# Kernel tuning notes

Measured on AMD Instinct MI355X. Metric: run time of the kernel, lower is better.

The kernel has to match this reference:

```python
import jax, jax.numpy as jnp
import numpy as np

B, S, DIM, HEADS, DHEAD = 1, 1992, 2048, 16, 128
NKI_SEQ_ALIGN = 128
EPS = 1e-6


def setup_inputs() -> dict:
    key = jax.random.key(0)
    ks = jax.random.split(key, 8)
    hidden_states = jax.random.normal(ks[0], (B, S, DIM), dtype=jnp.float32)
    # realistic rotary tables, full head_dim with interleaved pair angles
    pos = jnp.arange(S, dtype=jnp.float32)
    inv_freq = 1.0 / (10000.0 ** (jnp.arange(0, DHEAD, 2, dtype=jnp.float32) / DHEAD))
    ang = pos[:, None] * inv_freq[None, :]                      # [S, DHEAD/2]
    full = jnp.stack([ang, ang], axis=-1).reshape(S, DHEAD)     # interleave
    freqs_cos = jnp.cos(full)[None, :, None, :]                 # [1,S,1,DHEAD]
    freqs_sin = jnp.sin(full)[None, :, None, :]
    sc = 0.02
    wq = jax.random.normal(ks[1], (DIM, DIM), dtype=jnp.float32) * sc
    wk = jax.random.normal(ks[2], (DIM, DIM), dtype=jnp.float32) * sc
    wv = jax.random.normal(ks[3], (DIM, DIM), dtype=jnp.float32) * sc
    wo = jax.random.normal(ks[4], (DIM, DIM), dtype=jnp.float32) * sc
    bq = jax.random.normal(ks[5], (DIM,), dtype=jnp.float32) * sc
    bk = jax.random.normal(ks[6], (DIM,), dtype=jnp.float32) * sc
    bv = jax.random.normal(ks[7], (DIM,), dtype=jnp.float32) * sc
    bo = jnp.zeros((DIM,), dtype=jnp.float32)
    norm_q_w = jnp.ones((DIM,), dtype=jnp.float32)
    norm_k_w = jnp.ones((DIM,), dtype=jnp.float32)
    return dict(hidden_states=hidden_states, freqs_cos=freqs_cos, freqs_sin=freqs_sin,
                wq=wq, bq=bq, wk=wk, bk=bk, wv=wv, bv=bv,
                norm_q_w=norm_q_w, norm_k_w=norm_k_w, wo=wo, bo=bo)


def _rms_norm(x, weight, eps=EPS):
    xf = x.astype(jnp.float32)
    var = jnp.mean(xf * xf, axis=-1, keepdims=True)
    return (weight * (xf * jax.lax.rsqrt(var + eps))).astype(x.dtype)


def _apply_rope(x, freqs_cos, freqs_sin):
    # x: [B,H,S,D]; freqs: [1,S,1,D]
    cos = jnp.transpose(freqs_cos[..., 0::2], (0, 2, 1, 3))  # [1,1,S,D/2]
    sin = jnp.transpose(freqs_sin[..., 1::2], (0, 2, 1, 3))
    x1, x2 = x[..., 0::2], x[..., 1::2]
    o1 = x1 * cos - x2 * sin
    o2 = x1 * sin + x2 * cos
    return jnp.stack([o1, o2], axis=-1).reshape(x.shape)


def _attention_padded(q, k, v):
    # Faithful to nki_flash_attention: zero-pad seq to multiple of 128,
    # no masking of padded keys (they contribute logit 0), trim query pad.
    B_, H_, S_, D_ = q.shape
    pad = (-S_) % NKI_SEQ_ALIGN
    if pad:
        pc = [(0, 0), (0, 0), (0, pad), (0, 0)]
        q = jnp.pad(q, pc); k = jnp.pad(k, pc); v = jnp.pad(v, pc)
    scale = 1.0 / np.sqrt(D_)
    scores = jnp.einsum('bhqd,bhkd->bhqk', q, k) * scale
    probs = jax.nn.softmax(scores, axis=-1)
    out = jnp.einsum('bhqk,bhkd->bhqd', probs, v)
    return out[:, :, :S_, :]


def reference(hidden_states, freqs_cos, freqs_sin, wq, bq, wk, bk, wv, bv,
              norm_q_w, norm_k_w, wo, bo):
    b, s, _ = hidden_states.shape
    q = hidden_states @ wq.T + bq
    k = hidden_states @ wk.T + bk
    v = hidden_states @ wv.T + bv
    q = _rms_norm(q, norm_q_w)
    k = _rms_norm(k, norm_k_w)
    hd = q.shape[-1] // HEADS
    q = q.reshape(b, s, HEADS, hd).transpose(0, 2, 1, 3)
    k = k.reshape(b, s, HEADS, hd).transpose(0, 2, 1, 3)
    v = v.reshape(b, s, HEADS, hd).transpose(0, 2, 1, 3)
    q = _apply_rope(q, freqs_cos, freqs_sin)
    k = _apply_rope(k, freqs_cos, freqs_sin)
    o = _attention_padded(q, k, v)
    o = o.transpose(0, 2, 1, 3).reshape(b, s, -1)
    return o @ wo.T + bo
```

## Files before the change

kernel.cpp:

```cpp
#include <hip/hip_runtime.h>
#include <cstdint>

#define S_REAL 1992
#define S_PAD  2048
#define DIMSZ  2048
#define NHEAD  16
#define DHD    128

typedef float f32x4 __attribute__((ext_vector_type(4)));
typedef __bf16 bf16x8 __attribute__((ext_vector_type(8)));
typedef unsigned short u16x8 __attribute__((ext_vector_type(8)));

__device__ __forceinline__ unsigned short f2bf(float f){
  uint32_t u = __float_as_uint(f);
  u += 0x7fffu + ((u >> 16) & 1u);
  return (unsigned short)(u >> 16);
}

__device__ __forceinline__ void gload16(const void* g, void* l){
  __builtin_amdgcn_global_load_lds(
      (const __attribute__((address_space(1))) uint32_t*)g,
      (__attribute__((address_space(3))) uint32_t*)l,
      16, 0, 0);
}

template<int N> __device__ __forceinline__ void waitbar(){
  if constexpr (N == 8)      asm volatile("s_waitcnt vmcnt(8)\n\ts_barrier" ::: "memory");
  else if constexpr (N == 6) asm volatile("s_waitcnt vmcnt(6)\n\ts_barrier" ::: "memory");
  else if constexpr (N == 4) asm volatile("s_waitcnt vmcnt(4)\n\ts_barrier" ::: "memory");
  else if constexpr (N == 3) asm volatile("s_waitcnt vmcnt(3)\n\ts_barrier" ::: "memory");
  else                       asm volatile("s_waitcnt vmcnt(0)\n\ts_barrier" ::: "memory");
}

__launch_bounds__(256)
__global__ void k_cvt(const float* __restrict__ src, unsigned short* __restrict__ dst, int n8){
  int i = blockIdx.x * 256 + threadIdx.x;
  if (i >= n8) return;
  const float4* s = (const float4*)src + (size_t)i * 2;
  float4 a = s[0], b = s[1];
  u16x8 o;
  o[0]=f2bf(a.x); o[1]=f2bf(a.y); o[2]=f2bf(a.z); o[3]=f2bf(a.w);
  o[4]=f2bf(b.x); o[5]=f2bf(b.y); o[6]=f2bf(b.z); o[7]=f2bf(b.w);
  *((u16x8*)dst + i) = o;
}

template<int BN>
__launch_bounds__(512, 2)
__global__ void k_gemm8(const unsigned short* __restrict__ A,
                        const unsigned short* __restrict__ B0,
                        const unsigned short* __restrict__ B1,
                        const unsigned short* __restrict__ B2,
                        const float* __restrict__ bias0,
                        const float* __restrict__ bias1,
                        const float* __restrict__ bias2,
                        float* __restrict__ C0, float* __restrict__ C1, float* __restrict__ C2,
                        int Mreal)
{
  constexpr int WN   = BN / 64;
  constexpr int RM   = 256 / (8 / WN);
  constexpr int MI   = RM / 16;
  constexpr int NL   = (256 + BN) / 128;
  constexpr int BUFE = (256 + BN) * 32;
  constexpr int NT   = DIMSZ / 32;

  __shared__ unsigned short lds[4 * BUFE];

  const unsigned short* Bm = (blockIdx.z == 0) ? B0 : ((blockIdx.z == 1) ? B1 : B2);
  const float* bias        = (blockIdx.z == 0) ? bias0 : ((blockIdx.z == 1) ? bias1 : bias2);
  float* C                 = (blockIdx.z == 0) ? C0 : ((blockIdx.z == 1) ? C1 : C2);

  const int tid = threadIdx.x;
  const int w = tid >> 6, l = tid & 63;
  const int lr = l & 15, lg = l >> 4;
  const int m0 = blockIdx.x * 256, n0 = blockIdx.y * BN;
  const int wr = (w / WN) * RM, wc = (w % WN) * 64;

  f32x4 acc[MI][4];
  #pragma unroll
  for (int mi = 0; mi < MI; ++mi)
    #pragma unroll
    for (int ni = 0; ni < 4; ++ni)
      acc[mi][ni] = (f32x4){0.f, 0.f, 0.f, 0.f};

#define G8_STAGE(TT) do{                                                          \
    const int k0s = (TT) * 32;                                                    \
    unsigned short* dst = &lds[((TT) & 3) * BUFE];                                \
    _Pragma("unroll")                                                             \
    for (int i_ = 0; i_ < 2; ++i_){                                               \
      int lin = i_ * 512 + tid;                                                   \
      int r_ = lin >> 2, pos_ = lin & 3;                                          \
      int gr_ = m0 + r_; if (gr_ > Mreal - 1) gr_ = Mreal - 1;                    \
      gload16(A + (size_t)gr_ * DIMSZ + k0s + (pos_ ^ ((r_ >> 1) & 3)) * 8,       \
              dst + lin * 8);                                                     \
    }                                                                             \
    _Pragma("unroll")                                                             \
    for (int i_ = 0; i_ < BN / 128; ++i_){                                        \
      int lin = i_ * 512 + tid;                                                   \
      int r_ = lin >> 2, pos_ = lin & 3;                                          \
      gload16(Bm + (size_t)(n0 + r_) * DIMSZ + k0s + (pos_ ^ ((r_ >> 1) & 3)) * 8,\
              dst + 8192 + lin * 8);                                              \
    }                                                                             \
  } while(0)

#define G8_COMPUTE(TT) do{                                                        \
    const unsigned short* sb = &lds[((TT) & 3) * BUFE];                           \
    bf16x8 af_[MI]; bf16x8 bf_[4];                                                \
    _Pragma("unroll")                                                             \
    for (int mi = 0; mi < MI; ++mi){                                              \
      int r_ = wr + mi * 16 + lr;                                                 \
      af_[mi] = *(const bf16x8*)(sb + r_ * 32 + (lg ^ ((r_ >> 1) & 3)) * 8);      \
    }                                                                             \
    _Pragma("unroll")                                                             \
    for (int ni = 0; ni < 4; ++ni){                                               \
      int r_ = wc + ni * 16 + lr;                                                 \
      bf_[ni] = *(const bf16x8*)(sb + 8192 + r_ * 32 + (lg ^ ((r_ >> 1) & 3)) * 8);\
    }                                                                             \
    __builtin_amdgcn_s_setprio(1);                                                \
    _Pragma("unroll")                                                             \
    for (int mi = 0; mi < MI; ++mi)                                               \
      _Pragma("unroll")                                                           \
      for (int ni = 0; ni < 4; ++ni)                                              \
        acc[mi][ni] = __builtin_amdgcn_mfma_f32_16x16x32_bf16(af_[mi], bf_[ni],   \
                                                              acc[mi][ni], 0, 0, 0);\
    __builtin_amdgcn_s_setprio(0);                                                \
  } while(0)

  G8_STAGE(0); G8_STAGE(1); G8_STAGE(2);

  for (int tt = 0; tt < NT - 3; ++tt){
    waitbar<2 * NL>();
    G8_STAGE(tt + 3);
    G8_COMPUTE(tt);
  }
  waitbar<2 * NL>(); G8_COMPUTE(NT - 3);
  waitbar<NL>();     G8_COMPUTE(NT - 2);
  waitbar<0>();      G8_COMPUTE(NT - 1);

#undef G8_STAGE
#undef G8_COMPUTE

  #pragma unroll
  for (int ni = 0; ni < 4; ++ni){
    int col = n0 + wc + ni * 16 + lr;
    float bz = bias[col];
    #pragma unroll
    for (int mi = 0; mi < MI; ++mi){
      #pragma unroll
      for (int j = 0; j < 4; ++j){
        int row = m0 + wr + mi * 16 + lg * 4 + j;
        if (row < Mreal) C[(size_t)row * DIMSZ + col] = acc[mi][ni][j] + bz;
      }
    }
  }
}

__launch_bounds__(256)
__global__ void k_normrope(const float* __restrict__ Xf, const float* __restrict__ nw,
                           const float* __restrict__ fc, const float* __restrict__ fs,
                           unsigned short* __restrict__ Out, float scale, int swz)
{
  const int s = blockIdx.x;
  const int t = threadIdx.x;
  const int w = t >> 6, l = t & 63;
  __shared__ float wred[4];
  float v[8];
  float ss = 0.f;
  if (s < S_REAL){
    const float4* p = (const float4*)(Xf + (size_t)s * DIMSZ) + t * 2;
    float4 a = p[0], b = p[1];
    v[0]=a.x; v[1]=a.y; v[2]=a.z; v[3]=a.w; v[4]=b.x; v[5]=b.y; v[6]=b.z; v[7]=b.w;
    #pragma unroll
    for (int j = 0; j < 8; ++j) ss += v[j] * v[j];
  }
  #pragma unroll
  for (int off = 32; off >= 1; off >>= 1) ss += __shfl_xor(ss, off);
  if (l == 0) wred[w] = ss;
  __syncthreads();
  float tot = wred[0] + wred[1] + wred[2] + wred[3];
  float rinv = rsqrtf(tot * (1.f / DIMSZ) + 1e-6f);

  const int h  = t >> 4;
  const int d0 = (t & 15) * 8;
  const int b  = t & 15;
  const int bsw = swz ? (b ^ (s & 7)) : b;
  unsigned short* dst = Out + ((size_t)h * S_PAD + s) * DHD + bsw * 8;
  u16x8 o;
  if (s < S_REAL){
    #pragma unroll
    for (int i = 0; i < 4; ++i){
      float c_ = fc[s * DHD + d0 + 2 * i];
      float s_ = fs[s * DHD + d0 + 2 * i + 1];
      float x1 = v[2 * i]     * rinv * nw[t * 8 + 2 * i];
      float x2 = v[2 * i + 1] * rinv * nw[t * 8 + 2 * i + 1];
      o[2 * i]     = f2bf((x1 * c_ - x2 * s_) * scale);
      o[2 * i + 1] = f2bf((x1 * s_ + x2 * c_) * scale);
    }
  } else {
    #pragma unroll
    for (int j = 0; j < 8; ++j) o[j] = 0;
  }
  *(u16x8*)dst = o;
}

__launch_bounds__(256)
__global__ void k_vtrans(const float* __restrict__ Vf, unsigned short* __restrict__ Vth)
{
  __shared__ unsigned short tile[64][72];
  const int t = threadIdx.x;
  const int s0 = blockIdx.x * 64, c0 = blockIdx.y * 64;
  #pragma unroll
  for (int i = 0; i < 4; ++i){
    int r = (t >> 4) * 4 + i;
    int s = s0 + r;
    int cq = (t & 15) * 4;
    float4 val = {0.f, 0.f, 0.f, 0.f};
    if (s < S_REAL) val = *((const float4*)(Vf + (size_t)s * DIMSZ + c0) + (t & 15));
    tile[r][cq + 0] = f2bf(val.x);
    tile[r][cq + 1] = f2bf(val.y);
    tile[r][cq + 2] = f2bf(val.z);
    tile[r][cq + 3] = f2bf(val.w);
  }
  __syncthreads();
  const int cl = t >> 2;
  const int cc = c0 + cl;
  #pragma unroll
  for (int bi = 0; bi < 2; ++bi){
    int b = (t & 3) * 2 + bi;
    u16x8 o;
    #pragma unroll
    for (int j = 0; j < 8; ++j) o[j] = tile[b * 8 + j][cl];
    int bsw = b ^ (cc & 7);
    *(u16x8*)(Vth + (size_t)cc * S_PAD + s0 + bsw * 8) = o;
  }
}

__launch_bounds__(256)
__global__ void k_attn(const unsigned short* __restrict__ Qh,
                       const unsigned short* __restrict__ Kh,
                       const unsigned short* __restrict__ Vth,
                       unsigned short* __restrict__ O)
{
  __shared__ unsigned short kbuf[64 * 128];
  __shared__ unsigned short vbuf[128 * 64];
  __shared__ unsigned short pbuf[4][16 * 64];
  const int h = blockIdx.y;
  const int q0 = blockIdx.x * 64;
  const int t = threadIdx.x, w = t >> 6, l = t & 63;
  const int lr = l & 15, lg = l >> 4;

  const unsigned short* Qp = Qh + ((size_t)h * S_PAD + q0 + w * 16 + lr) * DHD;
  bf16x8 qf[4];
  #pragma unroll
  for (int ks = 0; ks < 4; ++ks) qf[ks] = *(const bf16x8*)(Qp + ks * 32 + lg * 8);

  f32x4 acc[8];
  #pragma unroll
  for (int nf = 0; nf < 8; ++nf) acc[nf] = (f32x4){0.f, 0.f, 0.f, 0.f};
  float m[4], lsum[4];
  #pragma unroll
  for (int j = 0; j < 4; ++j){ m[j] = -3.0e38f; lsum[j] = 0.f; }

  for (int kt = 0; kt < S_PAD / 64; ++kt){
    __syncthreads();
    #pragma unroll
    for (int i = 0; i < 4; ++i){
      int rK = (w * 4 + i) * 4 + (l >> 4);
      gload16(Kh + ((size_t)h * S_PAD + kt * 64 + rK) * DHD + (l & 15) * 8, &kbuf[(w * 4 + i) * 512]);
      int rV = (w * 4 + i) * 8 + (l >> 3);
      gload16(Vth + ((size_t)h * DHD + rV) * S_PAD + kt * 64 + (l & 7) * 8, &vbuf[(w * 4 + i) * 512]);
    }
    __syncthreads();

    f32x4 sf[4];
    #pragma unroll
    for (int kvf = 0; kvf < 4; ++kvf){
      sf[kvf] = (f32x4){0.f, 0.f, 0.f, 0.f};
      int r = kvf * 16 + lr;
      #pragma unroll
      for (int ks = 0; ks < 4; ++ks){
        int blk = (ks * 4 + lg) ^ (r & 7);
        bf16x8 kf = *(const bf16x8*)&kbuf[r * 128 + blk * 8];
        sf[kvf] = __builtin_amdgcn_mfma_f32_16x16x32_bf16(qf[ks], kf, sf[kvf], 0, 0, 0);
      }
    }

    float rowmax[4], rowsum[4], fr[4];
    #pragma unroll
    for (int j = 0; j < 4; ++j)
      rowmax[j] = fmaxf(fmaxf(sf[0][j], sf[1][j]), fmaxf(sf[2][j], sf[3][j]));
    #pragma unroll
    for (int off = 1; off <= 8; off <<= 1)
      #pragma unroll
      for (int j = 0; j < 4; ++j) rowmax[j] = fmaxf(rowmax[j], __shfl_xor(rowmax[j], off));
    #pragma unroll
    for (int j = 0; j < 4; ++j){
      float mn = fmaxf(m[j], rowmax[j]);
      fr[j] = __expf(m[j] - mn);
      m[j] = mn;
    }
    float p[4][4];
    #pragma unroll
    for (int kvf = 0; kvf < 4; ++kvf)
      #pragma unroll
      for (int j = 0; j < 4; ++j) p[kvf][j] = __expf(sf[kvf][j] - m[j]);
    #pragma unroll
    for (int j = 0; j < 4; ++j) rowsum[j] = p[0][j] + p[1][j] + p[2][j] + p[3][j];
    #pragma unroll
    for (int off = 1; off <= 8; off <<= 1)
      #pragma unroll
      for (int j = 0; j < 4; ++j) rowsum[j] += __shfl_xor(rowsum[j], off);
    f32x4 fv = (f32x4){fr[0], fr[1], fr[2], fr[3]};
    #pragma unroll
    for (int j = 0; j < 4; ++j) lsum[j] = lsum[j] * fr[j] + rowsum[j];
    #pragma unroll
    for (int nf = 0; nf < 8; ++nf) acc[nf] *= fv;

    unsigned short* pb = pbuf[w];
    #pragma unroll
    for (int kvf = 0; kvf < 4; ++kvf)
      #pragma unroll
      for (int j = 0; j < 4; ++j){
        int r = lg * 4 + j;
        int c = kvf * 16 + lr;
        int blk = (c >> 3) ^ (r & 7);
        pb[r * 64 + blk * 8 + (c & 7)] = f2bf(p[kvf][j]);
      }

    bf16x8 pf[2];
    #pragma unroll
    for (int ks = 0; ks < 2; ++ks){
      int blk = (ks * 4 + lg) ^ (lr & 7);
      pf[ks] = *(const bf16x8*)&pb[lr * 64 + blk * 8];
    }
    #pragma unroll
    for (int nf = 0; nf < 8; ++nf){
      int c = nf * 16 + lr;
      #pragma unroll
      for (int ks = 0; ks < 2; ++ks){
        int blk = (ks * 4 + lg) ^ (c & 7);
        bf16x8 vf = *(const bf16x8*)&vbuf[c * 64 + blk * 8];
        acc[nf] = __builtin_amdgcn_mfma_f32_16x16x32_bf16(pf[ks], vf, acc[nf], 0, 0, 0);
      }
    }
  }

  #pragma unroll
  for (int nf = 0; nf < 8; ++nf){
    #pragma unroll
    for (int j = 0; j < 4; ++j){
      int row = q0 + w * 16 + lg * 4 + j;
      if (row < S_REAL)
        O[(size_t)row * DIMSZ + h * DHD + nf * 16 + lr] = f2bf(acc[nf][j] / lsum[j]);
    }
  }
}

extern "C" void kernel_launch(void* const* d_in, const int* in_sizes, int n_in,
                              void* d_out, int out_size, void* d_ws, size_t ws_size,
                              hipStream_t stream)
{
  const float* hidden = (const float*)d_in[0];
  const float* fc  = (const float*)d_in[1];
  const float* fs  = (const float*)d_in[2];
  const float* wq  = (const float*)d_in[3];
  const float* bq  = (const float*)d_in[4];
  const float* wk  = (const float*)d_in[5];
  const float* bk  = (const float*)d_in[6];
  const float* wv  = (const float*)d_in[7];
  const float* bv  = (const float*)d_in[8];
  const float* nqw = (const float*)d_in[9];
  const float* nkw = (const float*)d_in[10];
  const float* wo  = (const float*)d_in[11];
  const float* bo  = (const float*)d_in[12];
  float* out = (float*)d_out;

  char* ws = (char*)d_ws;
  size_t off = 0;
  auto alloc = [&](size_t bytes) -> void* {
    void* p = ws + off;
    off += (bytes + 255) & ~(size_t)255;
    return p;
  };
  unsigned short* Xb  = (unsigned short*)alloc((size_t)S_REAL * DIMSZ * 2);
  unsigned short* Wqb = (unsigned short*)alloc((size_t)DIMSZ * DIMSZ * 2);
  unsigned short* Wkb = (unsigned short*)alloc((size_t)DIMSZ * DIMSZ * 2);
  unsigned short* Wvb = (unsigned short*)alloc((size_t)DIMSZ * DIMSZ * 2);
  unsigned short* Wob = (unsigned short*)alloc((size_t)DIMSZ * DIMSZ * 2);
  float* Qf = (float*)alloc((size_t)S_REAL * DIMSZ * 4);
  float* Kf = (float*)alloc((size_t)S_REAL * DIMSZ * 4);
  float* Vf = (float*)alloc((size_t)S_REAL * DIMSZ * 4);
  unsigned short* Qhh = (unsigned short*)alloc((size_t)NHEAD * S_PAD * DHD * 2);
  unsigned short* Khh = (unsigned short*)alloc((size_t)NHEAD * S_PAD * DHD * 2);
  unsigned short* Vth = (unsigned short*)alloc((size_t)NHEAD * DHD * S_PAD * 2);
  unsigned short* Oa  = (unsigned short*)alloc((size_t)S_REAL * DIMSZ * 2);

  k_cvt<<<S_REAL * DIMSZ / 8 / 256, 256, 0, stream>>>(hidden, Xb, S_REAL * DIMSZ / 8);
  k_cvt<<<DIMSZ * DIMSZ / 8 / 256, 256, 0, stream>>>(wq, Wqb, DIMSZ * DIMSZ / 8);
  k_cvt<<<DIMSZ * DIMSZ / 8 / 256, 256, 0, stream>>>(wk, Wkb, DIMSZ * DIMSZ / 8);
  k_cvt<<<DIMSZ * DIMSZ / 8 / 256, 256, 0, stream>>>(wv, Wvb, DIMSZ * DIMSZ / 8);
  k_cvt<<<DIMSZ * DIMSZ / 8 / 256, 256, 0, stream>>>(wo, Wob, DIMSZ * DIMSZ / 8);

  k_gemm8<256><<<dim3(8, 8, 3), 512, 0, stream>>>(Xb, Wqb, Wkb, Wvb, bq, bk, bv,
                                                  Qf, Kf, Vf, S_REAL);

  k_normrope<<<S_PAD, 256, 0, stream>>>(Qf, nqw, fc, fs, Qhh, 0.08838834764831843f, 0);
  k_normrope<<<S_PAD, 256, 0, stream>>>(Kf, nkw, fc, fs, Khh, 1.0f, 1);

  k_vtrans<<<dim3(S_PAD / 64, DIMSZ / 64), 256, 0, stream>>>(Vf, Vth);

  k_attn<<<dim3(S_PAD / 64, NHEAD), 256, 0, stream>>>(Qhh, Khh, Vth, Oa);

  k_gemm8<128><<<dim3(8, 16, 1), 512, 0, stream>>>(Oa, Wob, Wob, Wob, bo, bo, bo,
                                                   out, out, out, S_REAL);
}
```

Baseline: 256.0 us.

## Double-buffer attention K/V loads, transpose QK MFMA, retile output GEMM

The attention kernel now double-buffers K and V tiles in shared memory, prefetching the next tile while the current one is computed, so only one barrier per iteration remains. The QK MFMA operands are swapped, which transposes the score layout so each lane owns one query row's max and sum, cutting the shuffle reductions. P is written to LDS with packed 8-byte stores, and MFMA sections get raised priority. The GEMM gains a BM template parameter, and the output projection uses 128x128 tiles over 256 blocks to improve occupancy, at the cost of more redundant loads of A and B.

Result: faster. 218.6 us (-14.6%).

```diff
diff --git a/kernel.cpp b/kernel.cpp
--- a/kernel.cpp
+++ b/kernel.cpp
@@ -29,6 +29,7 @@
   else if constexpr (N == 6) asm volatile("s_waitcnt vmcnt(6)\n\ts_barrier" ::: "memory");
   else if constexpr (N == 4) asm volatile("s_waitcnt vmcnt(4)\n\ts_barrier" ::: "memory");
   else if constexpr (N == 3) asm volatile("s_waitcnt vmcnt(3)\n\ts_barrier" ::: "memory");
+  else if constexpr (N == 2) asm volatile("s_waitcnt vmcnt(2)\n\ts_barrier" ::: "memory");
   else                       asm volatile("s_waitcnt vmcnt(0)\n\ts_barrier" ::: "memory");
 }
 
@@ -44,7 +45,7 @@
   *((u16x8*)dst + i) = o;
 }
 
-template<int BN>
+template<int BM, int BN>
 __launch_bounds__(512, 2)
 __global__ void k_gemm8(const unsigned short* __restrict__ A,
                         const unsigned short* __restrict__ B0,
@@ -57,10 +58,12 @@
                         int Mreal)
 {
   constexpr int WN   = BN / 64;
-  constexpr int RM   = 256 / (8 / WN);
+  constexpr int WM   = 8 / WN;
+  constexpr int RM   = BM / WM;
   constexpr int MI   = RM / 16;
-  constexpr int NL   = (256 + BN) / 128;
-  constexpr int BUFE = (256 + BN) * 32;
+  constexpr int NL   = (BM + BN) / 128;
+  constexpr int BUFE = (BM + BN) * 32;
+  constexpr int BOFF = BM * 32;
   constexpr int NT   = DIMSZ / 32;
 
   __shared__ unsigned short lds[4 * BUFE];
@@ -72,7 +75,7 @@
   const int tid = threadIdx.x;
   const int w = tid >> 6, l = tid & 63;
   const int lr = l & 15, lg = l >> 4;
-  const int m0 = blockIdx.x * 256, n0 = blockIdx.y * BN;
+  const int m0 = blockIdx.x * BM, n0 = blockIdx.y * BN;
   const int wr = (w / WN) * RM, wc = (w % WN) * 64;
 
   f32x4 acc[MI][4];
@@ -86,7 +89,7 @@
     const int k0s = (TT) * 32;                                                    \
     unsigned short* dst = &lds[((TT) & 3) * BUFE];                                \
     _Pragma("unroll")                                                             \
-    for (int i_ = 0; i_ < 2; ++i_){                                               \
+    for (int i_ = 0; i_ < BM / 128; ++i_){                                        \
       int lin = i_ * 512 + tid;                                                   \
       int r_ = lin >> 2, pos_ = lin & 3;                                          \
       int gr_ = m0 + r_; if (gr_ > Mreal - 1) gr_ = Mreal - 1;                    \
@@ -98,7 +101,7 @@
       int lin = i_ * 512 + tid;                                                   \
       int r_ = lin >> 2, pos_ = lin & 3;                                          \
       gload16(Bm + (size_t)(n0 + r_) * DIMSZ + k0s + (pos_ ^ ((r_ >> 1) & 3)) * 8,\
-              dst + 8192 + lin * 8);                                              \
+              dst + BOFF + lin * 8);                                              \
     }                                                                             \
   } while(0)
 
@@ -113,7 +116,7 @@
     _Pragma("unroll")                                                             \
     for (int ni = 0; ni < 4; ++ni){                                               \
       int r_ = wc + ni * 16 + lr;                                                 \
-      bf_[ni] = *(const bf16x8*)(sb + 8192 + r_ * 32 + (lg ^ ((r_ >> 1) & 3)) * 8);\
+      bf_[ni] = *(const bf16x8*)(sb + BOFF + r_ * 32 + (lg ^ ((r_ >> 1) & 3)) * 8);\
     }                                                                             \
     __builtin_amdgcn_s_setprio(1);                                                \
     _Pragma("unroll")                                                             \
@@ -240,8 +243,8 @@
                        const unsigned short* __restrict__ Vth,
                        unsigned short* __restrict__ O)
 {
-  __shared__ unsigned short kbuf[64 * 128];
-  __shared__ unsigned short vbuf[128 * 64];
+  __shared__ unsigned short kbuf[2][64 * 128];
+  __shared__ unsigned short vbuf[2][128 * 64];
   __shared__ unsigned short pbuf[4][16 * 64];
   const int h = blockIdx.y;
   const int q0 = blockIdx.x * 64;
@@ -256,22 +259,29 @@
   f32x4 acc[8];
   #pragma unroll
   for (int nf = 0; nf < 8; ++nf) acc[nf] = (f32x4){0.f, 0.f, 0.f, 0.f};
-  float m[4], lsum[4];
-  #pragma unroll
-  for (int j = 0; j < 4; ++j){ m[j] = -3.0e38f; lsum[j] = 0.f; }
+  float m = -3.0e38f, lsum = 0.f;
+
+#define ATT_STAGE(KT, BI) do{                                                       \
+    _Pragma("unroll")                                                               \
+    for (int i_ = 0; i_ < 4; ++i_){                                                 \
+      int rK = (w * 4 + i_) * 4 + (l >> 4);                                         \
+      gload16(Kh + ((size_t)h * S_PAD + (KT) * 64 + rK) * DHD + (l & 15) * 8,       \
+              &kbuf[BI][(w * 4 + i_) * 512]);                                       \
+      int rV = (w * 4 + i_) * 8 + (l >> 3);                                         \
+      gload16(Vth + ((size_t)h * DHD + rV) * S_PAD + (KT) * 64 + (l & 7) * 8,       \
+              &vbuf[BI][(w * 4 + i_) * 512]);                                       \
+    }                                                                               \
+  } while(0)
+
+  ATT_STAGE(0, 0);
+  __syncthreads();
 
   for (int kt = 0; kt < S_PAD / 64; ++kt){
-    __syncthreads();
-    #pragma unroll
-    for (int i = 0; i < 4; ++i){
-      int rK = (w * 4 + i) * 4 + (l >> 4);
-      gload16(Kh + ((size_t)h * S_PAD + kt * 64 + rK) * DHD + (l & 15) * 8, &kbuf[(w * 4 + i) * 512]);
-      int rV = (w * 4 + i) * 8 + (l >> 3);
-      gload16(Vth + ((size_t)h * DHD + rV) * S_PAD + kt * 64 + (l & 7) * 8, &vbuf[(w * 4 + i) * 512]);
-    }
-    __syncthreads();
+    const int bi = kt & 1;
+    if (kt < S_PAD / 64 - 1) ATT_STAGE(kt + 1, bi ^ 1);
 
     f32x4 sf[4];
+    __builtin_amdgcn_s_setprio(1);
     #pragma unroll
     for (int kvf = 0; kvf < 4; ++kvf){
       sf[kvf] = (f32x4){0.f, 0.f, 0.f, 0.f};
@@ -279,70 +289,76 @@
       #pragma unroll
       for (int ks = 0; ks < 4; ++ks){
         int blk = (ks * 4 + lg) ^ (r & 7);
-        bf16x8 kf = *(const bf16x8*)&kbuf[r * 128 + blk * 8];
-        sf[kvf] = __builtin_amdgcn_mfma_f32_16x16x32_bf16(qf[ks], kf, sf[kvf], 0, 0, 0);
+        bf16x8 kf = *(const bf16x8*)&kbuf[bi][r * 128 + blk * 8];
+        sf[kvf] = __builtin_amdgcn_mfma_f32_16x16x32_bf16(kf, qf[ks], sf[kvf], 0, 0, 0);
       }
     }
-
-    float rowmax[4], rowsum[4], fr[4];
-    #pragma unroll
-    for (int j = 0; j < 4; ++j)
-      rowmax[j] = fmaxf(fmaxf(sf[0][j], sf[1][j]), fmaxf(sf[2][j], sf[3][j]));
-    #pragma unroll
-    for (int off = 1; off <= 8; off <<= 1)
-      #pragma unroll
-      for (int j = 0; j < 4; ++j) rowmax[j] = fmaxf(rowmax[j], __shfl_xor(rowmax[j], off));
-    #pragma unroll
-    for (int j = 0; j < 4; ++j){
-      float mn = fmaxf(m[j], rowmax[j]);
-      fr[j] = __expf(m[j] - mn);
-      m[j] = mn;
-    }
-    float p[4][4];
+    __builtin_amdgcn_s_setprio(0);
+
+    float pmax = sf[0][0];
     #pragma unroll
     for (int kvf = 0; kvf < 4; ++kvf)
       #pragma unroll
-      for (int j = 0; j < 4; ++j) p[kvf][j] = __expf(sf[kvf][j] - m[j]);
-    #pragma unroll
-    for (int j = 0; j < 4; ++j) rowsum[j] = p[0][j] + p[1][j] + p[2][j] + p[3][j];
-    #pragma unroll
-    for (int off = 1; off <= 8; off <<= 1)
-      #pragma unroll
-      for (int j = 0; j < 4; ++j) rowsum[j] += __shfl_xor(rowsum[j], off);
-    f32x4 fv = (f32x4){fr[0], fr[1], fr[2], fr[3]};
-    #pragma unroll
-    for (int j = 0; j < 4; ++j) lsum[j] = lsum[j] * fr[j] + rowsum[j];
-    #pragma unroll
-    for (int nf = 0; nf < 8; ++nf) acc[nf] *= fv;
-
-    unsigned short* pb = pbuf[w];
+      for (int j = 0; j < 4; ++j) pmax = fmaxf(pmax, sf[kvf][j]);
+    pmax = fmaxf(pmax, __shfl_xor(pmax, 16));
+    pmax = fmaxf(pmax, __shfl_xor(pmax, 32));
+    float mn = fmaxf(m, pmax);
+    float fr = __expf(m - mn);
+    m = mn;
+    float p[4][4];
+    float psum = 0.f;
     #pragma unroll
     for (int kvf = 0; kvf < 4; ++kvf)
       #pragma unroll
-      for (int j = 0; j < 4; ++j){
-        int r = lg * 4 + j;
-        int c = kvf * 16 + lr;
-        int blk = (c >> 3) ^ (r & 7);
-        pb[r * 64 + blk * 8 + (c & 7)] = f2bf(p[kvf][j]);
-      }
-
+      for (int j = 0; j < 4; ++j){ p[kvf][j] = __expf(sf[kvf][j] - mn); psum += p[kvf][j]; }
+    lsum = lsum * fr + psum;
+
+    float fv0 = __shfl(fr, lg * 4 + 0);
+    float fv1 = __shfl(fr, lg * 4 + 1);
+    float fv2 = __shfl(fr, lg * 4 + 2);
+    float fv3 = __shfl(fr, lg * 4 + 3);
+    f32x4 fv = (f32x4){fv0, fv1, fv2, fv3};
+    #pragma unroll
+    for (int nf = 0; nf < 8; ++nf) acc[nf] *= fv;
+
+    char* pb = (char*)pbuf[w];
+    #pragma unroll
+    for (int kvf = 0; kvf < 4; ++kvf){
+      uint2 wv;
+      wv.x = (uint32_t)f2bf(p[kvf][0]) | ((uint32_t)f2bf(p[kvf][1]) << 16);
+      wv.y = (uint32_t)f2bf(p[kvf][2]) | ((uint32_t)f2bf(p[kvf][3]) << 16);
+      int byte = lr * 128 + (((kvf * 2 + (lg >> 1)) ^ (lr & 7)) * 16) + (lg & 1) * 8;
+      *(uint2*)(pb + byte) = wv;
+    }
     bf16x8 pf[2];
     #pragma unroll
-    for (int ks = 0; ks < 2; ++ks){
-      int blk = (ks * 4 + lg) ^ (lr & 7);
-      pf[ks] = *(const bf16x8*)&pb[lr * 64 + blk * 8];
-    }
+    for (int c = 0; c < 2; ++c)
+      pf[c] = *(const bf16x8*)(pb + lr * 128 + ((c * 4 + lg) ^ (lr & 7)) * 16);
+
+    __builtin_amdgcn_s_setprio(1);
     #pragma unroll
     for (int nf = 0; nf < 8; ++nf){
-      int c = nf * 16 + lr;
+      int cc = nf * 16 + lr;
       #pragma unroll
       for (int ks = 0; ks < 2; ++ks){
-        int blk = (ks * 4 + lg) ^ (c & 7);
-        bf16x8 vf = *(const bf16x8*)&vbuf[c * 64 + blk * 8];
+        int blk = (ks * 4 + lg) ^ (cc & 7);
+        bf16x8 vf = *(const bf16x8*)&vbuf[bi][cc * 64 + blk * 8];
         acc[nf] = __builtin_amdgcn_mfma_f32_16x16x32_bf16(pf[ks], vf, acc[nf], 0, 0, 0);
       }
     }
-  }
+    __builtin_amdgcn_s_setprio(0);
+
+    __syncthreads();
+  }
+#undef ATT_STAGE
+
+  lsum += __shfl_xor(lsum, 16);
+  lsum += __shfl_xor(lsum, 32);
+  float ls0 = __shfl(lsum, lg * 4 + 0);
+  float ls1 = __shfl(lsum, lg * 4 + 1);
+  float ls2 = __shfl(lsum, lg * 4 + 2);
+  float ls3 = __shfl(lsum, lg * 4 + 3);
+  f32x4 lsv = (f32x4){1.f / ls0, 1.f / ls1, 1.f / ls2, 1.f / ls3};
 
   #pragma unroll
   for (int nf = 0; nf < 8; ++nf){
@@ -350,7 +366,7 @@
     for (int j = 0; j < 4; ++j){
       int row = q0 + w * 16 + lg * 4 + j;
       if (row < S_REAL)
-        O[(size_t)row * DIMSZ + h * DHD + nf * 16 + lr] = f2bf(acc[nf][j] / lsum[j]);
+        O[(size_t)row * DIMSZ + h * DHD + nf * 16 + lr] = f2bf(acc[nf][j] * lsv[j]);
     }
   }
 }
@@ -400,8 +416,8 @@
   k_cvt<<<DIMSZ * DIMSZ / 8 / 256, 256, 0, stream>>>(wv, Wvb, DIMSZ * DIMSZ / 8);
   k_cvt<<<DIMSZ * DIMSZ / 8 / 256, 256, 0, stream>>>(wo, Wob, DIMSZ * DIMSZ / 8);
 
-  k_gemm8<256><<<dim3(8, 8, 3), 512, 0, stream>>>(Xb, Wqb, Wkb, Wvb, bq, bk, bv,
-                                                  Qf, Kf, Vf, S_REAL);
+  k_gemm8<256, 256><<<dim3(8, 8, 3), 512, 0, stream>>>(Xb, Wqb, Wkb, Wvb, bq, bk, bv,
+                                                       Qf, Kf, Vf, S_REAL);
 
   k_normrope<<<S_PAD, 256, 0, stream>>>(Qf, nqw, fc, fs, Qhh, 0.08838834764831843f, 0);
   k_normrope<<<S_PAD, 256, 0, stream>>>(Kf, nkw, fc, fs, Khh, 1.0f, 1);
@@ -410,6 +426,6 @@
 
   k_attn<<<dim3(S_PAD / 64, NHEAD), 256, 0, stream>>>(Qhh, Khh, Vth, Oa);
 
-  k_gemm8<128><<<dim3(8, 16, 1), 512, 0, stream>>>(Oa, Wob, Wob, Wob, bo, bo, bo,
-                                                   out, out, out, S_REAL);
-}
+  k_gemm8<128, 128><<<dim3(16, 16, 1), 512, 0, stream>>>(Oa, Wob, Wob, Wob, bo, bo, bo,
+                                                         out, out, out, S_REAL);
+}
```
